# Kernel tuning notes

Measured on AMD Instinct MI355X. Metric: run time of the kernel, lower is better.

## Reference

```python
import jax, jax.numpy as jnp
import numpy as np

VOCAB, IMG_EMB, EMB, HID, P = 10000, 1024, 512, 512, 49
B, T = 64, 50


def setup_inputs() -> dict:
    key = jax.random.key(0)
    ks = jax.random.split(key, 16)
    def lin(k, fin, fout):
        k1, k2 = jax.random.split(k)
        s = 1.0 / np.sqrt(fin)
        return (jax.random.uniform(k1, (fin, fout), minval=-s, maxval=s),
                jax.random.uniform(k2, (fout,), minval=-s, maxval=s))
    Wv, bv = lin(ks[0], IMG_EMB, EMB)
    Wh, bh = lin(ks[1], EMB, HID)
    Wm, bm = lin(ks[2], EMB, HID)
    Wl, bl = lin(ks[3], 2 * EMB + HID, 5 * HID)  # LSTM fc on cat([w_t, vg, h])
    Wav, bav = lin(ks[4], HID, HID)
    Wah, bah = lin(ks[5], HID, HID)
    Was, bas = lin(ks[6], HID, HID)
    Waz, baz = lin(ks[7], HID, 1)
    Wp, bp = lin(ks[8], HID, VOCAB)
    emb = jax.random.normal(ks[9], (VOCAB, EMB)) * 0.02
    return {
        'v': jax.random.normal(ks[10], (B, P, IMG_EMB)),
        'w': jax.random.randint(ks[11], (B, T), 0, VOCAB),
        'lengths': jax.random.randint(ks[12], (B,), 0, T),
        'emb': emb,
        'Wv': Wv, 'bv': bv, 'Wh': Wh, 'bh': bh, 'Wm': Wm, 'bm': bm,
        'Wl': Wl, 'bl': bl,
        'Wav': Wav, 'bav': bav, 'Wah': Wah, 'bah': bah,
        'Was': Was, 'bas': bas, 'Waz': Waz, 'baz': baz,
        'Wp': Wp, 'bp': bp,
    }


def reference(v, w, lengths, emb, Wv, bv, Wh, bh, Wm, bm, Wl, bl,
              Wav, bav, Wah, bah, Was, bas, Waz, baz, Wp, bp):
    we = emb[w]                        # [B,T,E] word embeddings
    v = v @ Wv + bv                    # [B,P,E] projected visual features
    vg = v.mean(axis=1)                # [B,E] global visual feature
    h0 = vg @ Wh + bh                  # [B,H]
    m0 = vg @ Wm + bm                  # [B,H]
    pv = v @ Wav + bav                 # precompute attention proj of v [B,P,H]

    def step(carry, wt):
        h_, m_ = carry
        x = jnp.concatenate([wt, vg, h_], axis=-1)        # [B, 2E+H]
        i, f, o, g, m5 = jnp.split(x @ Wl + bl, 5, axis=-1)
        i = jax.nn.sigmoid(i)
        f = jax.nn.sigmoid(f)
        o = jax.nn.sigmoid(o)
        m = i * jnp.tanh(m5) + f * m_
        tm = jnp.tanh(m)
        h = o * tm
        s = g * tm                                        # sentinel gate
        # adaptive attention over P regions + sentinel h slot
        ph = (h @ Wah + bah)[:, None, :]                  # [B,1,H]
        ps = (s @ Was + bas)[:, None, :]                  # [B,1,H]
        z = jnp.tanh(jnp.concatenate([pv, ph], axis=1) + ps)  # [B,P+1,H]
        a = jax.nn.softmax(z @ Waz + baz, axis=1)         # [B,P+1,1]
        c = jnp.sum(a * jnp.concatenate([v, h[:, None, :]], axis=1), axis=1)
        p = jax.nn.softmax((c + h) @ Wp + bp, axis=-1)    # [B,V]
        return (h, m), p

    _, ps = jax.lax.scan(step, (h0, m0), jnp.swapaxes(we, 0, 1))
    ps = jnp.swapaxes(ps, 0, 1)                           # [B,T,V]
    mask = jnp.arange(ps.shape[1])[None, :] < lengths[:, None]
    return ps * mask[..., None].astype(ps.dtype)
```

## Files before the change

kernel.cpp:

```cpp
#include <hip/hip_runtime.h>
#include <hip/hip_bf16.h>
#include <cstdint>
#include <cstddef>

#define Bn 64
#define Tn 50
#define Pn 49
#define En 512
#define Hn 512
#define Vn 10000
#define IEn 1024
#define G5 2560

typedef __attribute__((ext_vector_type(8))) short bf16x8;
typedef __attribute__((ext_vector_type(4))) float f32x4;

typedef const __attribute__((address_space(1))) unsigned int* gptr_t;
typedef __attribute__((address_space(3))) unsigned int* lptr_t;

__device__ __forceinline__ float sigm(float x)  { return 1.0f / (1.0f + __expf(-x)); }
__device__ __forceinline__ float tanh_f(float x){ return 1.0f - 2.0f / (1.0f + __expf(2.0f * x)); }

__device__ __forceinline__ unsigned short f2b(float f) {
    union { float f; unsigned int u; } c; c.f = f;
    unsigned int u = c.u;
    u += 0x7fffu + ((u >> 16) & 1u);
    return (unsigned short)(u >> 16);
}
__device__ __forceinline__ float b2f(unsigned short u) {
    union { unsigned int u; float f; } c; c.u = ((unsigned int)u) << 16;
    return c.f;
}

template<bool GATHER>
__global__ __launch_bounds__(256)
void gemm64(const float* __restrict__ A, int lda,
            const float* __restrict__ B,
            float* __restrict__ C,
            int M, int N, int K,
            const float* __restrict__ bias,
            const float* __restrict__ rowadd, int rowDiv, long rowStride,
            const int* __restrict__ gidx)
{
    const int n0 = blockIdx.x * 64;
    const int m0 = blockIdx.y * 64;
    const long koff = (long)blockIdx.z * K;
    const float* Bp = B + koff * N;
    float* Cp = C + (gridDim.z > 1 ? (size_t)blockIdx.z * (size_t)M * (size_t)N : (size_t)0);

    __shared__ float As[16][64];
    __shared__ float Bs[16][64];

    const int tid = threadIdx.x;
    const int tx = tid & 15;
    const int ty = tid >> 4;
    const int ra = tid >> 2;
    const int ca = (tid & 3) << 2;

    long arow = GATHER ? (long)gidx[m0 + ra] : (long)(m0 + ra);
    const float* Arow = A + arow * (long)lda + koff + ca;

    const int kl = ty;
    const int nb = tx << 2;
    const int ncol = n0 + nb;

    float acc[4][4] = {{0.f,0.f,0.f,0.f},{0.f,0.f,0.f,0.f},{0.f,0.f,0.f,0.f},{0.f,0.f,0.f,0.f}};

    for (int k0 = 0; k0 < K; k0 += 16) {
        float4 av = *(const float4*)(Arow + k0);
        float4 bv;
        const float* bptr = Bp + (long)(k0 + kl) * N + ncol;
        if (ncol + 3 < N) {
            bv = *(const float4*)bptr;
        } else {
            bv.x = (ncol + 0 < N) ? bptr[0] : 0.f;
            bv.y = (ncol + 1 < N) ? bptr[1] : 0.f;
            bv.z = (ncol + 2 < N) ? bptr[2] : 0.f;
            bv.w = (ncol + 3 < N) ? bptr[3] : 0.f;
        }
        __syncthreads();
        As[ca + 0][ra] = av.x; As[ca + 1][ra] = av.y;
        As[ca + 2][ra] = av.z; As[ca + 3][ra] = av.w;
        *(float4*)&Bs[kl][nb] = bv;
        __syncthreads();
        #pragma unroll
        for (int kk = 0; kk < 16; kk++) {
            const float4 a = *(const float4*)&As[kk][ty << 2];
            const float4 b = *(const float4*)&Bs[kk][tx << 2];
            const float a_[4] = {a.x, a.y, a.z, a.w};
            const float b_[4] = {b.x, b.y, b.z, b.w};
            #pragma unroll
            for (int i = 0; i < 4; i++)
                #pragma unroll
                for (int j = 0; j < 4; j++)
                    acc[i][j] = fmaf(a_[i], b_[j], acc[i][j]);
        }
    }

    #pragma unroll
    for (int i = 0; i < 4; i++) {
        const int rr = m0 + (ty << 2) + i;
        #pragma unroll
        for (int j = 0; j < 4; j++) {
            const int cc = n0 + (tx << 2) + j;
            if (cc < N) {
                float v = acc[i][j];
                if (bias)   v += bias[cc];
                if (rowadd) v += rowadd[(long)(rr / rowDiv) * rowStride + cc];
                Cp[(long)rr * N + cc] = v;
            }
        }
    }
}

template<int OUTF, int OUTB, int GM, int SWZ>
__global__ __launch_bounds__(256)
void gemm_mfma(const unsigned short* __restrict__ A,
               const unsigned short* __restrict__ BT,
               float* __restrict__ Cf, unsigned short* __restrict__ Cb,
               int M, int N, int K,
               const float* __restrict__ bias,
               const float* __restrict__ rowadd, int rowDiv,
               const int* __restrict__ ridx, const int* __restrict__ dcnt,
               int mtiles)
{
    __shared__ __align__(16) unsigned short Asm[128 * 32];
    __shared__ __align__(16) unsigned short Bsm[128 * 32];

    int Meff = M;
    if (GM) Meff = *dcnt;
    int m0, n0;
    if (SWZ) {
        const int nwg = gridDim.x;
        const int q = nwg >> 3, rm = nwg & 7;
        const int xcd = blockIdx.x & 7, pos = blockIdx.x >> 3;
        const int swz = (xcd < rm ? xcd * (q + 1) : rm * (q + 1) + (xcd - rm) * q) + pos;
        m0 = (swz % mtiles) * 128;
        n0 = (swz / mtiles) * 128;
    } else {
        n0 = blockIdx.x * 128;
        m0 = blockIdx.y * 128;
    }
    if (GM && m0 >= Meff) return;

    const int tid = threadIdx.x;
    const int lane = tid & 63;
    const int wv = tid >> 6;
    const int wm = wv >> 1;
    const int wn = wv & 1;

    const int srow = lane >> 2;
    const int kg8 = (lane & 3) * 8;
    const int arA0 = m0 + wv * 16 + srow, arA1 = arA0 + 64;
    const int brB0 = n0 + wv * 16 + srow, brB1 = brB0 + 64;
    long arow0, arow1;
    if (GM) {
        arow0 = (arA0 < Meff) ? (long)ridx[arA0] : 0;
        arow1 = (arA1 < Meff) ? (long)ridx[arA1] : 0;
    } else {
        arow0 = arA0; arow1 = arA1;
    }

    lptr_t ldsA0 = (lptr_t)&Asm[(size_t)wv * 512];
    lptr_t ldsA1 = (lptr_t)&Asm[(size_t)(wv + 4) * 512];
    lptr_t ldsB0 = (lptr_t)&Bsm[(size_t)wv * 512];
    lptr_t ldsB1 = (lptr_t)&Bsm[(size_t)(wv + 4) * 512];

    f32x4 acc[4][4] = {};

    const int arowf = wm * 64 + (lane & 15);
    const int browf = wn * 64 + (lane & 15);
    const int kcol = (lane >> 4) * 8;

    for (int k0 = 0; k0 < K; k0 += 32) {
        __syncthreads();
        {
            const long ka = (long)k0 + kg8;
            __builtin_amdgcn_global_load_lds((gptr_t)(A + arow0 * K + ka), ldsA0, 16, 0, 0);
            __builtin_amdgcn_global_load_lds((gptr_t)(A + arow1 * K + ka), ldsA1, 16, 0, 0);
            __builtin_amdgcn_global_load_lds((gptr_t)(BT + (long)brB0 * K + ka), ldsB0, 16, 0, 0);
            __builtin_amdgcn_global_load_lds((gptr_t)(BT + (long)brB1 * K + ka), ldsB1, 16, 0, 0);
        }
        __syncthreads();

        bf16x8 af[4], bfr[4];
        #pragma unroll
        for (int i = 0; i < 4; i++) {
            af[i]  = *(const bf16x8*)&Asm[(arowf + i * 16) * 32 + kcol];
            bfr[i] = *(const bf16x8*)&Bsm[(browf + i * 16) * 32 + kcol];
        }
        #pragma unroll
        for (int mi = 0; mi < 4; mi++)
            #pragma unroll
            for (int ni = 0; ni < 4; ni++)
                acc[mi][ni] = __builtin_amdgcn_mfma_f32_16x16x32_bf16(af[mi], bfr[ni], acc[mi][ni], 0, 0, 0);
    }

    const int crow = m0 + wm * 64 + (lane >> 4) * 4;
    const int ccol0 = n0 + wn * 64 + (lane & 15);
    #pragma unroll
    for (int ni = 0; ni < 4; ni++) {
        const int col = ccol0 + ni * 16;
        if (col >= N) continue;
        const float bvv = bias ? bias[col] : 0.f;
        #pragma unroll
        for (int mi = 0; mi < 4; mi++) {
            #pragma unroll
            for (int r = 0; r < 4; r++) {
                const int rr = crow + mi * 16 + r;
                if (rr < Meff) {
                    const long orow = GM ? (long)ridx[rr] : (long)rr;
                    float v = acc[mi][ni][r] + bvv;
                    if (rowadd) v += rowadd[(orow / rowDiv) * N + col];
                    if (OUTF) Cf[orow * N + col] = v;
                    if (OUTB) Cb[orow * N + col] = f2b(v);
                }
            }
        }
    }
}

__global__ __launch_bounds__(256)
void transpose_bf16(const float* __restrict__ in, unsigned short* __restrict__ out,
                    int K, int N, int istride)
{
    __shared__ float tile[32][33];
    const int k0 = blockIdx.y * 32;
    const int n0 = blockIdx.x * 32;
    const int tx = threadIdx.x & 31, ty = threadIdx.x >> 5;
    #pragma unroll
    for (int j = 0; j < 4; j++) {
        int k = k0 + ty + j * 8, n = n0 + tx;
        tile[ty + j * 8][tx] = (k < K && n < N) ? in[(long)k * istride + n] : 0.f;
    }
    __syncthreads();
    #pragma unroll
    for (int j = 0; j < 4; j++) {
        int n = n0 + ty + j * 8, k = k0 + tx;
        if (n < N && k < K) out[(long)n * K + k] = f2b(tile[tx][ty + j * 8]);
    }
}

__global__ __launch_bounds__(256)
void transpose2_G5(const float* __restrict__ Wl,
                   unsigned short* __restrict__ O0, unsigned short* __restrict__ O1)
{
    const float* in = Wl + (blockIdx.z ? (size_t)1024 * G5 : (size_t)0);
    unsigned short* out = blockIdx.z ? O1 : O0;
    __shared__ float tile[32][33];
    const int k0 = blockIdx.y * 32;
    const int n0 = blockIdx.x * 32;
    const int tx = threadIdx.x & 31, ty = threadIdx.x >> 5;
    #pragma unroll
    for (int j = 0; j < 4; j++)
        tile[ty + j * 8][tx] = in[(long)(k0 + ty + j * 8) * G5 + n0 + tx];
    __syncthreads();
    #pragma unroll
    for (int j = 0; j < 4; j++)
        out[(long)(n0 + ty + j * 8) * 512 + k0 + tx] = f2b(tile[tx][ty + j * 8]);
}

__global__ __launch_bounds__(256)
void transpose3_bf16(const float* __restrict__ A0, const float* __restrict__ A1,
                     const float* __restrict__ A2,
                     unsigned short* __restrict__ O0, unsigned short* __restrict__ O1,
                     unsigned short* __restrict__ O2)
{
    const float* in = (blockIdx.z == 0) ? A0 : (blockIdx.z == 1) ? A1 : A2;
    unsigned short* out = (blockIdx.z == 0) ? O0 : (blockIdx.z == 1) ? O1 : O2;
    __shared__ float tile[32][33];
    const int k0 = blockIdx.y * 32;
    const int n0 = blockIdx.x * 32;
    const int tx = threadIdx.x & 31, ty = threadIdx.x >> 5;
    #pragma unroll
    for (int j = 0; j < 4; j++)
        tile[ty + j * 8][tx] = in[(long)(k0 + ty + j * 8) * 512 + n0 + tx];
    __syncthreads();
    #pragma unroll
    for (int j = 0; j < 4; j++)
        out[(long)(n0 + ty + j * 8) * 512 + k0 + tx] = f2b(tile[tx][ty + j * 8]);
}

__global__ void convert_bf16(const float* __restrict__ in, unsigned short* __restrict__ out, int n4)
{
    int i = blockIdx.x * 256 + threadIdx.x;
    if (i < n4) {
        float4 v = ((const float4*)in)[i];
        ushort4 u;
        u.x = f2b(v.x); u.y = f2b(v.y); u.z = f2b(v.z); u.w = f2b(v.w);
        ((ushort4*)out)[i] = u;
    }
}

__global__ void gather_convert(const float* __restrict__ emb, const int* __restrict__ w,
                               unsigned short* __restrict__ out)
{
    const int r = blockIdx.x;
    const long row = w[r];
    const float4 v = ((const float4*)(emb + row * 512))[threadIdx.x];
    ushort4 u;
    u.x = f2b(v.x); u.y = f2b(v.y); u.z = f2b(v.z); u.w = f2b(v.w);
    ((ushort4*)(out + (long)r * 512))[threadIdx.x] = u;
}

__global__ void compact_rows(const int* __restrict__ len, int* __restrict__ ridx, int* __restrict__ dcnt)
{
    const int b = threadIdx.x;
    int L = len[b]; L = L < 0 ? 0 : (L > Tn ? Tn : L);
    int off = L;
    #pragma unroll
    for (int s = 1; s < 64; s <<= 1) {
        int n = __shfl_up(off, s);
        if (b >= s) off += n;
    }
    const int start = off - L;
    if (b == 63) *dcnt = off;
    for (int t = 0; t < L; t++) ridx[start + t] = b * Tn + t;
}

__global__ void vg_mean(const unsigned short* __restrict__ vproj, float* __restrict__ vg)
{
    const int tid = blockIdx.x * 256 + threadIdx.x;
    const int b = tid >> 9, e = tid & 511;
    const unsigned short* p = vproj + (long)b * Pn * En + e;
    float s = 0.f;
    #pragma unroll 7
    for (int q = 0; q < Pn; q++) s += b2f(p[q * En]);
    vg[tid] = s * (1.0f / 49.0f);
}

__global__ void h0m0(const float* __restrict__ vg,
                     const float* __restrict__ Wh, const float* __restrict__ bh,
                     const float* __restrict__ Wm, const float* __restrict__ bm,
                     unsigned short* __restrict__ h0b, float* __restrict__ m)
{
    __shared__ float vgs[512];
    const int b = blockIdx.x, e = threadIdx.x;
    vgs[e] = vg[b * 512 + e];
    __syncthreads();
    float a1 = bh[e], a2 = bm[e];
    #pragma unroll 8
    for (int k = 0; k < 512; k++) {
        const float x = vgs[k];
        a1 = fmaf(x, Wh[(long)k * 512 + e], a1);
        a2 = fmaf(x, Wm[(long)k * 512 + e], a2);
    }
    h0b[b * 512 + e] = f2b(a1);
    m[b * 512 + e] = a2;
}

__global__ __launch_bounds__(256)
void scan_step(int t, const float* __restrict__ base,
               const unsigned short* __restrict__ hcur,
               unsigned short* __restrict__ hnxt,
               float* __restrict__ mF,
               const unsigned short* __restrict__ W3T,
               float* __restrict__ HsF, unsigned short* __restrict__ Hsb,
               unsigned short* __restrict__ Ssb)
{
    __shared__ __align__(16) unsigned short Wh_s[5][8][520];

    const int tid = threadIdx.x;
    const int lane = tid & 63, wv = tid >> 6;
    const int e0 = blockIdx.x * 8;
    const int col = lane & 15;
    const int fk = (lane >> 4) * 8;
    const int bb = wv * 16 + (lane & 15);

    bf16x8 Ah[16];
    #pragma unroll
    for (int ch = 0; ch < 16; ch++)
        Ah[ch] = *(const bf16x8*)(hcur + (long)bb * 512 + ch * 32 + fk);

    for (int idx = tid; idx < 40 * 64; idx += 256) {
        const int row = idx >> 6, seg = idx & 63;
        const int g = row >> 3, c = row & 7;
        *(uint4*)&Wh_s[g][c][seg * 8] =
            *(const uint4*)(W3T + (long)(g * 512 + e0 + c) * 512 + seg * 8);
    }

    const int rbase = wv * 16 + (lane >> 4) * 4;
    const int ecol = e0 + (col & 7);
    float bse[5][4], mv[4];
    if (col < 8) {
        #pragma unroll
        for (int r = 0; r < 4; r++) {
            const long rrow = (long)(rbase + r) * Tn + t;
            const float* bp = base + rrow * G5 + ecol;
            bse[0][r] = bp[0];    bse[1][r] = bp[512];  bse[2][r] = bp[1024];
            bse[3][r] = bp[1536]; bse[4][r] = bp[2048];
            mv[r] = mF[(rbase + r) * 512 + ecol];
        }
    }

    __syncthreads();

    const unsigned short* B0 = &Wh_s[(col >> 3)    ][col & 7][0];
    const unsigned short* B1 = &Wh_s[2 + (col >> 3)][col & 7][0];
    const unsigned short* B2 = &Wh_s[4][col & 7][0];

    f32x4 a0 = {}, a1 = {}, a2 = {};
    #pragma unroll
    for (int ch = 0; ch < 16; ch++) {
        const int ko = ch * 32 + fk;
        a0 = __builtin_amdgcn_mfma_f32_16x16x32_bf16(Ah[ch], *(const bf16x8*)(B0 + ko), a0, 0, 0, 0);
        a1 = __builtin_amdgcn_mfma_f32_16x16x32_bf16(Ah[ch], *(const bf16x8*)(B1 + ko), a1, 0, 0, 0);
        a2 = __builtin_amdgcn_mfma_f32_16x16x32_bf16(Ah[ch], *(const bf16x8*)(B2 + ko), a2, 0, 0, 0);
    }

    #pragma unroll
    for (int r = 0; r < 4; r++) {
        const float fsh = __shfl_xor(a0[r], 8);
        const float gsh = __shfl_xor(a1[r], 8);
        if (col < 8) {
            const int b = rbase + r;
            const float gi = a0[r] + bse[0][r];
            const float gf = fsh   + bse[1][r];
            const float go = a1[r] + bse[2][r];
            const float gg = gsh   + bse[3][r];
            const float g5 = a2[r] + bse[4][r];
            const float iv = sigm(gi), fv = sigm(gf), ov = sigm(go);
            const float mn = fmaf(iv, tanh_f(g5), fv * mv[r]);
            const float tm = tanh_f(mn);
            const float hh = ov * tm, ss = gg * tm;
            const unsigned short hhi = f2b(hh);
            const long hoff = (long)b * 512 + ecol;
            const long rrow = (long)b * Tn + t;
            mF[hoff] = mn;
            hnxt[hoff] = hhi;
            HsF[rrow * 512 + ecol] = hh;
            Hsb[rrow * 512 + ecol] = hhi;
            Ssb[rrow * 512 + ecol] = f2b(ss);
        }
    }
}

__global__ __launch_bounds__(256)
void attn(const unsigned short* __restrict__ vproj, const float* __restrict__ pv,
          const float* __restrict__ PH, const float* __restrict__ PS,
          const float* __restrict__ Hs, const float* __restrict__ Waz,
          const float* __restrict__ baz, unsigned short* __restrict__ CHb,
          const int* __restrict__ len)
{
    const int r = (blockIdx.x & 7) * 400 + (blockIdx.x >> 3);
    const int b = r / Tn;
    if ((r % Tn) >= len[b]) return;
    const int tid = threadIdx.x;
    const int lane = tid & 63, wid = tid >> 6;

    __shared__ float ps_s[512];
    __shared__ float ph_s[512];
    __shared__ float alog[64];

    for (int i = tid; i < 512; i += 256) {
        ps_s[i] = PS[(long)r * 512 + i];
        ph_s[i] = PH[(long)r * 512 + i];
    }
    __syncthreads();

    const float4 wz0 = *(const float4*)(Waz + lane * 8);
    const float4 wz1 = *(const float4*)(Waz + lane * 8 + 4);
    const float4 q0  = *(const float4*)&ps_s[lane * 8];
    const float4 q1  = *(const float4*)&ps_s[lane * 8 + 4];

    for (int slot = wid; slot < Pn + 1; slot += 4) {
        const float* src = (slot < Pn) ? (pv + ((long)b * Pn + slot) * 512)
                                       : (const float*)ph_s;
        const float4 x0 = *(const float4*)(src + lane * 8);
        const float4 x1 = *(const float4*)(src + lane * 8 + 4);
        float d = 0.f;
        d = fmaf(tanh_f(x0.x + q0.x), wz0.x, d);
        d = fmaf(tanh_f(x0.y + q0.y), wz0.y, d);
        d = fmaf(tanh_f(x0.z + q0.z), wz0.z, d);
        d = fmaf(tanh_f(x0.w + q0.w), wz0.w, d);
        d = fmaf(tanh_f(x1.x + q1.x), wz1.x, d);
        d = fmaf(tanh_f(x1.y + q1.y), wz1.y, d);
        d = fmaf(tanh_f(x1.z + q1.z), wz1.z, d);
        d = fmaf(tanh_f(x1.w + q1.w), wz1.w, d);
        #pragma unroll
        for (int s = 32; s >= 1; s >>= 1) d += __shfl_xor(d, s);
        if (lane == 0) alog[slot] = d + baz[0];
    }
    __syncthreads();

    if (wid == 0) {
        const float v = (lane < Pn + 1) ? alog[lane] : -3.4e38f;
        float mx = v;
        #pragma unroll
        for (int s = 32; s >= 1; s >>= 1) mx = fmaxf(mx, __shfl_xor(mx, s));
        const float ev = (lane < Pn + 1) ? __expf(v - mx) : 0.f;
        float sm = ev;
        #pragma unroll
        for (int s = 32; s >= 1; s >>= 1) sm += __shfl_xor(sm, s);
        if (lane < Pn + 1) alog[lane] = ev / sm;
    }
    __syncthreads();

    const float a49 = alog[Pn];
    for (int ee = tid; ee < 512; ee += 256) {
        const float hval = Hs[(long)r * 512 + ee];
        float c = a49 * hval;
        const unsigned short* vp = vproj + (long)b * Pn * 512 + ee;
        #pragma unroll 7
        for (int q = 0; q < Pn; q++) c = fmaf(alog[q], b2f(vp[q * 512]), c);
        CHb[(long)r * 512 + ee] = f2b(c + hval);
    }
}

__global__ __launch_bounds__(256)
void softmax_mask(float* __restrict__ out, const int* __restrict__ lengths)
{
    const int r = blockIdx.x, b = r / Tn, t = r % Tn;
    float* row = out + (long)r * Vn;
    const int tid = threadIdx.x;
    float4* row4 = (float4*)row;

    if (t >= lengths[b]) {
        f32x4* rowv = (f32x4*)row;
        const f32x4 z = {0.f, 0.f, 0.f, 0.f};
        for (int i = tid; i < Vn / 4; i += 256)
            __builtin_nontemporal_store(z, &rowv[i]);
        return;
    }

    __shared__ float red[4];
    const int lane = tid & 63, wid = tid >> 6;

    float4 rv[10];
    float mx = -3.4e38f;
    #pragma unroll
    for (int j = 0; j < 10; j++) {
        const int i = tid + j * 256;
        if (i < Vn / 4) {
            rv[j] = row4[i];
            mx = fmaxf(mx, fmaxf(fmaxf(rv[j].x, rv[j].y), fmaxf(rv[j].z, rv[j].w)));
        }
    }
    #pragma unroll
    for (int s = 32; s >= 1; s >>= 1) mx = fmaxf(mx, __shfl_xor(mx, s));
    if (lane == 0) red[wid] = mx;
    __syncthreads();
    mx = fmaxf(fmaxf(red[0], red[1]), fmaxf(red[2], red[3]));
    __syncthreads();

    float sm = 0.f;
    #pragma unroll
    for (int j = 0; j < 10; j++) {
        const int i = tid + j * 256;
        if (i < Vn / 4) {
            rv[j].x = __expf(rv[j].x - mx);
            rv[j].y = __expf(rv[j].y - mx);
            rv[j].z = __expf(rv[j].z - mx);
            rv[j].w = __expf(rv[j].w - mx);
            sm += rv[j].x + rv[j].y + rv[j].z + rv[j].w;
        }
    }
    #pragma unroll
    for (int s = 32; s >= 1; s >>= 1) sm += __shfl_xor(sm, s);
    if (lane == 0) red[wid] = sm;
    __syncthreads();
    sm = red[0] + red[1] + red[2] + red[3];
    const float inv = 1.0f / sm;

    #pragma unroll
    for (int j = 0; j < 10; j++) {
        const int i = tid + j * 256;
        if (i < Vn / 4) {
            rv[j].x *= inv; rv[j].y *= inv; rv[j].z *= inv; rv[j].w *= inv;
            row4[i] = rv[j];
        }
    }
}

extern "C" void kernel_launch(void* const* d_in, const int* in_sizes, int n_in,
                              void* d_out, int out_size, void* d_ws, size_t ws_size,
                              hipStream_t stream)
{
    (void)in_sizes; (void)n_in; (void)out_size; (void)ws_size;
    const float* v   = (const float*)d_in[0];
    const int*   w   = (const int*)  d_in[1];
    const int*   len = (const int*)  d_in[2];
    const float* emb = (const float*)d_in[3];
    const float* Wv  = (const float*)d_in[4];
    const float* bv  = (const float*)d_in[5];
    const float* Wh  = (const float*)d_in[6];
    const float* bh  = (const float*)d_in[7];
    const float* Wm  = (const float*)d_in[8];
    const float* bm  = (const float*)d_in[9];
    const float* Wl  = (const float*)d_in[10];
    const float* bl  = (const float*)d_in[11];
    const float* Wav = (const float*)d_in[12];
    const float* bav = (const float*)d_in[13];
    const float* Wah = (const float*)d_in[14];
    const float* bah = (const float*)d_in[15];
    const float* Was = (const float*)d_in[16];
    const float* bas = (const float*)d_in[17];
    const float* Waz = (const float*)d_in[18];
    const float* baz = (const float*)d_in[19];
    const float* Wp  = (const float*)d_in[20];
    const float* bp  = (const float*)d_in[21];
    float* out_f = (float*)d_out;

    char* wsp = (char*)d_ws;
    size_t off = 0;
    auto walloc = [&](size_t bytes) -> void* {
        void* r = wsp + off;
        off += (bytes + 255) & ~(size_t)255;
        return r;
    };
    unsigned short* WpT    = (unsigned short*)walloc((size_t)Vn * 512 * 2);
    unsigned short* WvT    = (unsigned short*)walloc((size_t)512 * 1024 * 2);
    unsigned short* WlT0   = (unsigned short*)walloc((size_t)G5 * 512 * 2);
    unsigned short* WavT   = (unsigned short*)walloc((size_t)512 * 512 * 2);
    unsigned short* WahT   = (unsigned short*)walloc((size_t)512 * 512 * 2);
    unsigned short* WasT   = (unsigned short*)walloc((size_t)512 * 512 * 2);
    unsigned short* vprojb = (unsigned short*)walloc((size_t)3136 * 512 * 2);
    unsigned short* CHb    = (unsigned short*)walloc((size_t)3200 * 512 * 2);
    float* vg   = (float*)walloc((size_t)64 * 512 * 4);
    unsigned short* hB = (unsigned short*)walloc((size_t)2 * 64 * 512 * 2);
    float* mbuf = (float*)walloc((size_t)64 * 512 * 4);
    float* vgw  = (float*)walloc((size_t)64 * G5 * 4);
    int*   ridx = (int*)walloc((size_t)3200 * 4);
    int*   dcnt = (int*)walloc(256);

    char* sp = (char*)(out_f + (size_t)3200 * G5);
    size_t off2 = 0;
    auto salloc = [&](size_t bytes) -> void* {
        void* r = sp + off2;
        off2 += (bytes + 255) & ~(size_t)255;
        return r;
    };
    unsigned short* vB  = (unsigned short*)salloc((size_t)3136 * 1024 * 2);
    unsigned short* WEb = (unsigned short*)salloc((size_t)3200 * 512 * 2);
    float* pvb = (float*)salloc((size_t)3136 * 512 * 4);
    float* HsF = (float*)salloc((size_t)3200 * 512 * 4);
    unsigned short* Hsb = (unsigned short*)salloc((size_t)3200 * 512 * 2);
    unsigned short* Ssb = (unsigned short*)salloc((size_t)3200 * 512 * 2);
    float* PHb = (float*)salloc((size_t)3200 * 512 * 4);
    float* PSb = (float*)salloc((size_t)3200 * 512 * 4);
    unsigned short* W3T = (unsigned short*)salloc((size_t)G5 * 512 * 2);

    transpose_bf16<<<dim3(512/32, 1024/32), 256, 0, stream>>>(Wv, WvT, 1024, 512, 512);
    transpose2_G5<<<dim3(G5/32, 16, 2), 256, 0, stream>>>(Wl, WlT0, W3T);
    transpose3_bf16<<<dim3(16, 16, 3), 256, 0, stream>>>(Wav, Wah, Was, WavT, WahT, WasT);
    transpose_bf16<<<dim3((Vn + 31)/32, 16), 256, 0, stream>>>(Wp, WpT, 512, Vn, Vn);
    convert_bf16<<<(3136*1024/4 + 255)/256, 256, 0, stream>>>(v, vB, 3136*1024/4);
    gather_convert<<<3200, 128, 0, stream>>>(emb, w, WEb);
    compact_rows<<<1, 64, 0, stream>>>(len, ridx, dcnt);

    gemm_mfma<0,1,0,0><<<dim3(4, 25), 256, 0, stream>>>(vB, WvT, nullptr, vprojb,
                                                        3136, 512, 1024, bv, nullptr, 1,
                                                        nullptr, nullptr, 0);
    vg_mean<<<128, 256, 0, stream>>>(vprojb, vg);
    h0m0<<<64, 512, 0, stream>>>(vg, Wh, bh, Wm, bm, hB, mbuf);
    gemm64<false><<<dim3(40, 1, 1), 256, 0, stream>>>(vg, 512, Wl + (size_t)512 * G5, vgw,
                                                      64, G5, 512, bl, nullptr, 1, 0, nullptr);
    gemm_mfma<1,0,0,0><<<dim3(4, 25), 256, 0, stream>>>(vprojb, WavT, pvb, nullptr,
                                                        3136, 512, 512, bav, nullptr, 1,
                                                        nullptr, nullptr, 0);
    gemm_mfma<1,0,0,1><<<500, 256, 0, stream>>>(WEb, WlT0, out_f, nullptr,
                                                3200, G5, 512, nullptr, vgw, Tn,
                                                nullptr, nullptr, 25);
    for (int t = 0; t < Tn; t++) {
        const size_t cur = (size_t)(t & 1) * (64 * 512);
        const size_t nxt = (size_t)((t + 1) & 1) * (64 * 512);
        scan_step<<<64, 256, 0, stream>>>(t, out_f, hB + cur, hB + nxt, mbuf, W3T,
                                          HsF, Hsb, Ssb);
    }
    gemm_mfma<1,0,1,0><<<dim3(4, 25), 256, 0, stream>>>(Hsb, WahT, PHb, nullptr,
                                                        3200, 512, 512, bah, nullptr, 1,
                                                        ridx, dcnt, 0);
    gemm_mfma<1,0,1,0><<<dim3(4, 25), 256, 0, stream>>>(Ssb, WasT, PSb, nullptr,
                                                        3200, 512, 512, bas, nullptr, 1,
                                                        ridx, dcnt, 0);
    attn<<<3200, 256, 0, stream>>>(vprojb, pvb, PHb, PSb, HsF, Waz, baz, CHb, len);
    gemm_mfma<1,0,1,1><<<1975, 256, 0, stream>>>(CHb, WpT, out_f, nullptr,
                                                 3200, Vn, 512, bp, nullptr, 1,
                                                 ridx, dcnt, 25);
    softmax_mask<<<3200, 256, 0, stream>>>(out_f, len);
}
```

Before: 812.1 us.

## Replace per-timestep scan launches with one persistent kernel using grid barrier

The 50 separate scan_step launches become a single persistent kernel of 64 blocks that loops over time steps. Each block loads its slice of the recurrent weights into LDS once, keeps the cell state in registers, and prefetches the next step's gate bases. Blocks synchronise through a global atomic counter barrier after every step. This removes per-launch overhead and repeated weight loads, but it relies on all 64 blocks being resident at once and adds atomic spin-wait latency at each step.

```diff
diff --git a/kernel.cpp b/kernel.cpp
--- a/kernel.cpp
+++ b/kernel.cpp
@@ -11,6 +11,7 @@
 #define Vn 10000
 #define IEn 1024
 #define G5 2560
+#define NBLK 64
 
 typedef __attribute__((ext_vector_type(8))) short bf16x8;
 typedef __attribute__((ext_vector_type(4))) float f32x4;
@@ -350,13 +351,13 @@
 }
 
 __global__ __launch_bounds__(256)
-void scan_step(int t, const float* __restrict__ base,
-               const unsigned short* __restrict__ hcur,
-               unsigned short* __restrict__ hnxt,
-               float* __restrict__ mF,
-               const unsigned short* __restrict__ W3T,
-               float* __restrict__ HsF, unsigned short* __restrict__ Hsb,
-               unsigned short* __restrict__ Ssb)
+void scan_persist(const float* __restrict__ base,
+                  unsigned short* __restrict__ hB,
+                  const float* __restrict__ m0,
+                  const unsigned short* __restrict__ W3T,
+                  float* __restrict__ HsF, unsigned short* __restrict__ Hsb,
+                  unsigned short* __restrict__ Ssb,
+                  int* __restrict__ bar)
 {
     __shared__ __align__(16) unsigned short Wh_s[5][8][520];
 
@@ -367,11 +368,6 @@
     const int fk = (lane >> 4) * 8;
     const int bb = wv * 16 + (lane & 15);
 
-    bf16x8 Ah[16];
-    #pragma unroll
-    for (int ch = 0; ch < 16; ch++)
-        Ah[ch] = *(const bf16x8*)(hcur + (long)bb * 512 + ch * 32 + fk);
-
     for (int idx = tid; idx < 40 * 64; idx += 256) {
         const int row = idx >> 6, seg = idx & 63;
         const int g = row >> 3, c = row & 7;
@@ -381,57 +377,99 @@
 
     const int rbase = wv * 16 + (lane >> 4) * 4;
     const int ecol = e0 + (col & 7);
-    float bse[5][4], mv[4];
+    float mreg[4];
     if (col < 8) {
         #pragma unroll
+        for (int r = 0; r < 4; r++)
+            mreg[r] = m0[(rbase + r) * 512 + ecol];
+    }
+
+    float bse[5][4];
+    if (col < 8) {
+        #pragma unroll
         for (int r = 0; r < 4; r++) {
-            const long rrow = (long)(rbase + r) * Tn + t;
-            const float* bp = base + rrow * G5 + ecol;
+            const float* bp = base + ((long)(rbase + r) * Tn + 0) * G5 + ecol;
             bse[0][r] = bp[0];    bse[1][r] = bp[512];  bse[2][r] = bp[1024];
             bse[3][r] = bp[1536]; bse[4][r] = bp[2048];
-            mv[r] = mF[(rbase + r) * 512 + ecol];
-        }
-    }
-
-    __syncthreads();
+        }
+    }
 
     const unsigned short* B0 = &Wh_s[(col >> 3)    ][col & 7][0];
     const unsigned short* B1 = &Wh_s[2 + (col >> 3)][col & 7][0];
     const unsigned short* B2 = &Wh_s[4][col & 7][0];
 
-    f32x4 a0 = {}, a1 = {}, a2 = {};
-    #pragma unroll
-    for (int ch = 0; ch < 16; ch++) {
-        const int ko = ch * 32 + fk;
-        a0 = __builtin_amdgcn_mfma_f32_16x16x32_bf16(Ah[ch], *(const bf16x8*)(B0 + ko), a0, 0, 0, 0);
-        a1 = __builtin_amdgcn_mfma_f32_16x16x32_bf16(Ah[ch], *(const bf16x8*)(B1 + ko), a1, 0, 0, 0);
-        a2 = __builtin_amdgcn_mfma_f32_16x16x32_bf16(Ah[ch], *(const bf16x8*)(B2 + ko), a2, 0, 0, 0);
-    }
-
-    #pragma unroll
-    for (int r = 0; r < 4; r++) {
-        const float fsh = __shfl_xor(a0[r], 8);
-        const float gsh = __shfl_xor(a1[r], 8);
+    __syncthreads();
+
+    for (int t = 0; t < Tn; t++) {
+        const unsigned short* hcur = hB + (size_t)(t & 1) * (64 * 512);
+        unsigned short* hnxt = hB + (size_t)((t + 1) & 1) * (64 * 512);
+
+        bf16x8 Ah[16];
+        #pragma unroll
+        for (int ch = 0; ch < 16; ch++)
+            Ah[ch] = *(const bf16x8*)(hcur + (long)bb * 512 + ch * 32 + fk);
+
+        f32x4 a0 = {}, a1 = {}, a2 = {};
+        #pragma unroll
+        for (int ch = 0; ch < 16; ch++) {
+            const int ko = ch * 32 + fk;
+            a0 = __builtin_amdgcn_mfma_f32_16x16x32_bf16(Ah[ch], *(const bf16x8*)(B0 + ko), a0, 0, 0, 0);
+            a1 = __builtin_amdgcn_mfma_f32_16x16x32_bf16(Ah[ch], *(const bf16x8*)(B1 + ko), a1, 0, 0, 0);
+            a2 = __builtin_amdgcn_mfma_f32_16x16x32_bf16(Ah[ch], *(const bf16x8*)(B2 + ko), a2, 0, 0, 0);
+        }
+
+        #pragma unroll
+        for (int r = 0; r < 4; r++) {
+            const float fsh = __shfl_xor(a0[r], 8);
+            const float gsh = __shfl_xor(a1[r], 8);
+            if (col < 8) {
+                const int b = rbase + r;
+                const float gi = a0[r] + bse[0][r];
+                const float gf = fsh   + bse[1][r];
+                const float go = a1[r] + bse[2][r];
+                const float gg = gsh   + bse[3][r];
+                const float g5 = a2[r] + bse[4][r];
+                const float iv = sigm(gi), fv = sigm(gf), ov = sigm(go);
+                const float mn = fmaf(iv, tanh_f(g5), fv * mreg[r]);
+                const float tm = tanh_f(mn);
+                const float hh = ov * tm, ss = gg * tm;
+                const unsigned short hhi = f2b(hh);
+                const long hoff = (long)b * 512 + ecol;
+                const long rrow = (long)b * Tn + t;
+                mreg[r] = mn;
+                hnxt[hoff] = hhi;
+                HsF[rrow * 512 + ecol] = hh;
+                Hsb[rrow * 512 + ecol] = hhi;
+                Ssb[rrow * 512 + ecol] = f2b(ss);
+            }
+        }
+
+        if (t + 1 >= Tn) break;
+
         if (col < 8) {
-            const int b = rbase + r;
-            const float gi = a0[r] + bse[0][r];
-            const float gf = fsh   + bse[1][r];
-            const float go = a1[r] + bse[2][r];
-            const float gg = gsh   + bse[3][r];
-            const float g5 = a2[r] + bse[4][r];
-            const float iv = sigm(gi), fv = sigm(gf), ov = sigm(go);
-            const float mn = fmaf(iv, tanh_f(g5), fv * mv[r]);
-            const float tm = tanh_f(mn);
-            const float hh = ov * tm, ss = gg * tm;
-            const unsigned short hhi = f2b(hh);
-            const long hoff = (long)b * 512 + ecol;
-            const long rrow = (long)b * Tn + t;
-            mF[hoff] = mn;
-            hnxt[hoff] = hhi;
-            HsF[rrow * 512 + ecol] = hh;
-            Hsb[rrow * 512 + ecol] = hhi;
-            Ssb[rrow * 512 + ecol] = f2b(ss);
-        }
+            #pragma unroll
+            for (int r = 0; r < 4; r++) {
+                const float* bp = base + ((long)(rbase + r) * Tn + (t + 1)) * G5 + ecol;
+                bse[0][r] = bp[0];    bse[1][r] = bp[512];  bse[2][r] = bp[1024];
+                bse[3][r] = bp[1536]; bse[4][r] = bp[2048];
+            }
+        }
+
+        __syncthreads();
+        if (tid == 0) {
+            __threadfence();
+            const int old = __hip_atomic_fetch_add(&bar[0], 1, __ATOMIC_ACQ_REL, __HIP_MEMORY_SCOPE_AGENT);
+            if (old == NBLK - 1) {
+                __hip_atomic_store(&bar[0], 0, __ATOMIC_RELAXED, __HIP_MEMORY_SCOPE_AGENT);
+                __hip_atomic_fetch_add(&bar[1], 1, __ATOMIC_RELEASE, __HIP_MEMORY_SCOPE_AGENT);
+            } else {
+                while (__hip_atomic_load(&bar[1], __ATOMIC_ACQUIRE, __HIP_MEMORY_SCOPE_AGENT) <= t) {
+                    __builtin_amdgcn_s_sleep(2);
+                }
+            }
+            __threadfence();
+        }
+        __syncthreads();
     }
 }
 
@@ -622,6 +660,7 @@
     float* vgw  = (float*)walloc((size_t)64 * G5 * 4);
     int*   ridx = (int*)walloc((size_t)3200 * 4);
     int*   dcnt = (int*)walloc(256);
+    int*   bar  = (int*)walloc(256);
 
     char* sp = (char*)(out_f + (size_t)3200 * G5);
     size_t off2 = 0;
@@ -640,6 +679,8 @@
     float* PSb = (float*)salloc((size_t)3200 * 512 * 4);
     unsigned short* W3T = (unsigned short*)salloc((size_t)G5 * 512 * 2);
 
+    hipMemsetAsync(bar, 0, 16, stream);
+
     transpose_bf16<<<dim3(512/32, 1024/32), 256, 0, stream>>>(Wv, WvT, 1024, 512, 512);
     transpose2_G5<<<dim3(G5/32, 16, 2), 256, 0, stream>>>(Wl, WlT0, W3T);
     transpose3_bf16<<<dim3(16, 16, 3), 256, 0, stream>>>(Wav, Wah, Was, WavT, WahT, WasT);
@@ -661,12 +702,7 @@
     gemm_mfma<1,0,0,1><<<500, 256, 0, stream>>>(WEb, WlT0, out_f, nullptr,
                                                 3200, G5, 512, nullptr, vgw, Tn,
                                                 nullptr, nullptr, 25);
-    for (int t = 0; t < Tn; t++) {
-        const size_t cur = (size_t)(t & 1) * (64 * 512);
-        const size_t nxt = (size_t)((t + 1) & 1) * (64 * 512);
-        scan_step<<<64, 256, 0, stream>>>(t, out_f, hB + cur, hB + nxt, mbuf, W3T,
-                                          HsF, Hsb, Ssb);
-    }
+    scan_persist<<<NBLK, 256, 0, stream>>>(out_f, hB, mbuf, W3T, HsF, Hsb, Ssb, bar);
     gemm_mfma<1,0,1,0><<<dim3(4, 25), 256, 0, stream>>>(Hsb, WahT, PHb, nullptr,
                                                         3200, 512, 512, bah, nullptr, 1,
                                                         ridx, dcnt, 0);
```

After: 980.0 us. 1.21x slower.
